# Kernel optimization log

Measured on AMD Instinct MI355X. Metric: run time of the kernel, lower is better.

The kernel has to match this reference:

```python
import jax, jax.numpy as jnp
import numpy as np

C = 256
NUM_HEADS = 8
NUM_GROUPS = 32
EPS = 1e-5


def setup_inputs() -> dict:
    key = jax.random.key(0)
    ks = jax.random.split(key, 7)
    B, H, W = 2, 64, 64
    x = jax.random.normal(ks[0], (B, C, H, W), dtype=jnp.float32)
    norm_gamma = jnp.ones((C,), dtype=jnp.float32)
    norm_beta = jnp.zeros((C,), dtype=jnp.float32)
    # 1x1 convs == per-pixel linear layers; store weights as (out_ch, in_ch)
    qkv_w = jax.random.normal(ks[1], (3 * C, C), dtype=jnp.float32) * (1.0 / np.sqrt(C))
    qkv_b = jnp.zeros((3 * C,), dtype=jnp.float32)
    proj_w = jax.random.normal(ks[2], (C, C), dtype=jnp.float32) * (1.0 / np.sqrt(C))
    proj_b = jnp.zeros((C,), dtype=jnp.float32)
    return {"x": x, "norm_gamma": norm_gamma, "norm_beta": norm_beta,
            "qkv_w": qkv_w, "qkv_b": qkv_b, "proj_w": proj_w, "proj_b": proj_b}


def _group_norm(x, gamma, beta):
    B, Cc, H, W = x.shape
    xg = x.reshape(B, NUM_GROUPS, Cc // NUM_GROUPS, H, W)
    mean = xg.mean(axis=(2, 3, 4), keepdims=True)
    var = xg.var(axis=(2, 3, 4), keepdims=True)
    xn = ((xg - mean) * jax.lax.rsqrt(var + EPS)).reshape(B, Cc, H, W)
    return xn * gamma[None, :, None, None] + beta[None, :, None, None]


def reference(x, norm_gamma, norm_beta, qkv_w, qkv_b, proj_w, proj_b):
    B, Cc, H, W = x.shape
    hd = Cc // NUM_HEADS
    N = H * W

    h = _group_norm(x, norm_gamma, norm_beta)
    # 1x1 conv: (3C,C) x (B,C,H,W) -> (B,3C,H,W)
    qkv = jnp.einsum('oc,bchw->bohw', qkv_w, h) + qkv_b[None, :, None, None]
    q, k, v = jnp.split(qkv, 3, axis=1)

    def heads(t):  # (B,C,H,W) -> (B,heads,N,hd)
        return t.reshape(B, NUM_HEADS, hd, N).transpose(0, 1, 3, 2)

    q, k, v = heads(q), heads(k), heads(v)
    scale = hd ** (-0.5)
    attn = jax.nn.softmax(jnp.einsum('bhnd,bhmd->bhnm', q, k) * scale, axis=-1)
    out = jnp.einsum('bhnm,bhmd->bhnd', attn, v)  # (B,heads,N,hd)
    out = out.transpose(0, 1, 3, 2).reshape(B, Cc, H, W)
    out = jnp.einsum('oc,bchw->bohw', proj_w, out) + proj_b[None, :, None, None]
    return x + out
```

## Files before the change

kernel.cpp:

```cpp
#include <hip/hip_runtime.h>
#include <math.h>

#define C_    256
#define NH    8
#define HD_   32
#define NG    32
#define CPG   8
#define NPIX  4096
#define BATCH 2
#define EPSV  1e-5f
#define SLOG2 0.25503489f
#define MF    16.0f
#define KVB   128
#define KSTR  40
#define VSTR  136
#define KPS2  2048

typedef __bf16 bf16x8 __attribute__((ext_vector_type(8)));
typedef __bf16 bf16x4 __attribute__((ext_vector_type(4)));
typedef float  f32x4  __attribute__((ext_vector_type(4)));

__global__ __launch_bounds__(256) void prep_kernel(const float* __restrict__ x,
                                                   float* __restrict__ partial,
                                                   const float* __restrict__ qw,
                                                   const float* __restrict__ pw,
                                                   __bf16* __restrict__ wbq,
                                                   __bf16* __restrict__ wbp) {
    if (blockIdx.x >= 512) {
        const int i = ((blockIdx.x - 512) * 256 + threadIdx.x) * 4;
        const float* src;
        __bf16* dst;
        int off;
        if (i < 768 * 256) { src = qw; dst = wbq; off = i; }
        else { src = pw; dst = wbp; off = i - 768 * 256; }
        const float4 v = *(const float4*)(src + off);
        bf16x4 o;
        o[0] = (__bf16)v.x; o[1] = (__bf16)v.y; o[2] = (__bf16)v.z; o[3] = (__bf16)v.w;
        *(bf16x4*)(dst + off) = o;
        return;
    }
    const int bg = blockIdx.x >> 3;
    const int part = blockIdx.x & 7;
    const int b = bg >> 5, g = bg & 31;
    const float* __restrict__ xp = x + ((size_t)(b * C_ + g * CPG)) * NPIX;

    float s = 0.f, ss = 0.f;
    #pragma unroll
    for (int p = 0; p < 4; ++p) {
        const int i = part * 4096 + p * 1024 + threadIdx.x * 4;
        const float4 v = *(const float4*)(xp + i);
        s  += v.x + v.y + v.z + v.w;
        ss += v.x * v.x + v.y * v.y + v.z * v.z + v.w * v.w;
    }
    #pragma unroll
    for (int off = 32; off; off >>= 1) {
        s  += __shfl_down(s, off);
        ss += __shfl_down(ss, off);
    }
    __shared__ float ls[4], lss[4];
    const int wid = threadIdx.x >> 6, lane = threadIdx.x & 63;
    if (lane == 0) { ls[wid] = s; lss[wid] = ss; }
    __syncthreads();
    if (threadIdx.x == 0) {
        float S = 0.f, SS = 0.f;
        #pragma unroll
        for (int w = 0; w < 4; ++w) { S += ls[w]; SS += lss[w]; }
        partial[bg * 16 + part * 2 + 0] = S;
        partial[bg * 16 + part * 2 + 1] = SS;
    }
}

__global__ __launch_bounds__(256) void qkv_gemm_kernel(const __bf16* __restrict__ wbq,
                                                       const float* __restrict__ bias,
                                                       const float* __restrict__ x,
                                                       const float* __restrict__ partial,
                                                       const float* __restrict__ gamma,
                                                       const float* __restrict__ beta,
                                                       __bf16* __restrict__ Qb,
                                                       __bf16* __restrict__ Kb,
                                                       __bf16* __restrict__ Vb) {
    const int b = blockIdx.z;
    const int n0 = blockIdx.x * 64;
    __shared__ __align__(16) __bf16 tile[64][264];
    __shared__ float gstat[NG][2];

    if (threadIdx.x < NG) {
        float S = 0.f, SS = 0.f;
        #pragma unroll
        for (int p = 0; p < 8; ++p) {
            S  += partial[(b * NG + threadIdx.x) * 16 + p * 2 + 0];
            SS += partial[(b * NG + threadIdx.x) * 16 + p * 2 + 1];
        }
        const float inv_n = 1.0f / (float)(CPG * NPIX);
        const float mean = S * inv_n;
        const float var  = SS * inv_n - mean * mean;
        gstat[threadIdx.x][0] = mean;
        gstat[threadIdx.x][1] = rsqrtf(var + EPSV);
    }
    __syncthreads();

    {
        const int nn = (threadIdx.x & 15) * 4;
        #pragma unroll
        for (int p = 0; p < 16; ++p) {
            const int c = (threadIdx.x >> 4) + p * 16;
            const float4 v = *(const float4*)(x + ((size_t)(b * C_ + c)) * NPIX + n0 + nn);
            const int g = c >> 3;
            const float ga = gamma[c] * gstat[g][1];
            const float be = beta[c] - gstat[g][0] * ga;
            tile[nn + 0][c] = (__bf16)(v.x * ga + be);
            tile[nn + 1][c] = (__bf16)(v.y * ga + be);
            tile[nn + 2][c] = (__bf16)(v.z * ga + be);
            tile[nn + 3][c] = (__bf16)(v.w * ga + be);
        }
    }
    __syncthreads();

    const int wave = threadIdx.x >> 6, lane = threadIdx.x & 63;
    const int col = lane & 15, g = lane >> 4;
    const int m0 = blockIdx.y * 128 + wave * 32;

    f32x4 acc[2][4];
    #pragma unroll
    for (int i = 0; i < 2; ++i)
        #pragma unroll
        for (int j = 0; j < 4; ++j) acc[i][j] = (f32x4){0.f, 0.f, 0.f, 0.f};

    #pragma unroll
    for (int c0 = 0; c0 < C_; c0 += 32) {
        bf16x8 la[2], lb[4];
        #pragma unroll
        for (int mb = 0; mb < 2; ++mb)
            la[mb] = *(const bf16x8*)(wbq + (size_t)(m0 + mb * 16 + col) * C_ + c0 + g * 8);
        #pragma unroll
        for (int nb = 0; nb < 4; ++nb)
            lb[nb] = *(const bf16x8*)(&tile[nb * 16 + col][c0 + g * 8]);
        #pragma unroll
        for (int mb = 0; mb < 2; ++mb)
            #pragma unroll
            for (int nb = 0; nb < 4; ++nb)
                acc[mb][nb] = __builtin_amdgcn_mfma_f32_16x16x32_bf16(la[mb], lb[nb], acc[mb][nb], 0, 0, 0);
    }

    #pragma unroll
    for (int mb = 0; mb < 2; ++mb) {
        const int mbase = m0 + mb * 16 + 4 * g;
        const float4 b4 = *(const float4*)(bias + mbase);
        const int route = mbase >> 8;
        const int bh = b * NH + ((mbase >> 5) & 7);
        const int d0 = mbase & 31;
        #pragma unroll
        for (int nb = 0; nb < 4; ++nb) {
            const int n = n0 + nb * 16 + col;
            f32x4 v = acc[mb][nb];
            v[0] += b4.x; v[1] += b4.y; v[2] += b4.z; v[3] += b4.w;
            if (route == 0) {
                bf16x4 o;
                #pragma unroll
                for (int r = 0; r < 4; ++r) o[r] = (__bf16)(v[r] * SLOG2);
                *(bf16x4*)(Qb + (((size_t)bh * NPIX + n) << 5) + d0) = o;
            } else if (route == 1) {
                bf16x4 o;
                #pragma unroll
                for (int r = 0; r < 4; ++r) o[r] = (__bf16)v[r];
                *(bf16x4*)(Kb + (((size_t)bh * NPIX + n) << 5) + d0) = o;
            } else {
                #pragma unroll
                for (int r = 0; r < 4; ++r)
                    Vb[((size_t)bh * HD_ + d0 + r) * NPIX + n] = (__bf16)v[r];
            }
        }
    }
}

__global__ __launch_bounds__(512) void attn_kernel(const __bf16* __restrict__ Qb,
                                                   const __bf16* __restrict__ Kb,
                                                   const __bf16* __restrict__ Vb,
                                                   __bf16* __restrict__ aot) {
    __shared__ __align__(16) char smem[75776];
    __bf16 (*Ks)[2][KVB][KSTR] = (__bf16 (*)[2][KVB][KSTR])(smem);
    __bf16 (*Vs)[2][HD_][VSTR] = (__bf16 (*)[2][HD_][VSTR])(smem + 40960);
    float* pbuf = (float*)smem;

    const int id = blockIdx.x;
    const int h = id & 7;
    const int rest = id >> 3;
    const int b = rest >> 5;
    const int qt = rest & 31;

    const int wave = threadIdx.x >> 6, lane = threadIdx.x & 63;
    const int hw = wave >> 2, wv = wave & 3;
    const int col = lane & 15, g = lane >> 4;
    const int bh = b * NH + h;
    const int q0 = qt * 128 + wv * 32;

    const __bf16* __restrict__ qp = Qb + ((size_t)bh * NPIX + q0) * HD_;
    const __bf16* __restrict__ kp = Kb + ((size_t)bh * NPIX + hw * KPS2) * HD_;
    const __bf16* __restrict__ vp = Vb + (size_t)bh * HD_ * NPIX + hw * KPS2;

    const int sk_key = wv * 16 + (lane >> 2);
    const int sk_seg = (lane & 3) * 8;
    const int sv_d   = wv * 8 + (lane >> 3);
    const int sv_seg = (lane & 7) * 8;
    const int vslot  = (sv_seg & 32) + ((((sv_seg & 15) >> 2) << 3)) + (((sv_seg >> 4) & 1) << 2);
    const __bf16* __restrict__ kg = kp + (size_t)sk_key * HD_ + sk_seg;
    const __bf16* __restrict__ vg = vp + (size_t)sv_d * NPIX + sv_seg;

    const bf16x8 fq0 = *(const bf16x8*)(qp + col * HD_ + g * 8);
    const bf16x8 fq1 = *(const bf16x8*)(qp + (16 + col) * HD_ + g * 8);

    bf16x8 ones;
    #pragma unroll
    for (int j = 0; j < 8; ++j) ones[j] = (__bf16)1.0f;
    const f32x4 mfc = {-MF, -MF, -MF, -MF};

    f32x4 acc00 = {0.f,0.f,0.f,0.f}, acc01 = {0.f,0.f,0.f,0.f};
    f32x4 acc10 = {0.f,0.f,0.f,0.f}, acc11 = {0.f,0.f,0.f,0.f};
    f32x4 accL0 = {0.f,0.f,0.f,0.f}, accL1 = {0.f,0.f,0.f,0.f};

    {
        const bf16x8 rk0 = *(const bf16x8*)(kg);
        const bf16x8 rk1 = *(const bf16x8*)(kg + (size_t)64 * HD_);
        const bf16x8 rv0 = *(const bf16x8*)(vg);
        const bf16x8 rv1 = *(const bf16x8*)(vg + 64);
        *(bf16x8*)&Ks[hw][0][sk_key][sk_seg]      = rk0;
        *(bf16x8*)&Ks[hw][0][sk_key + 64][sk_seg] = rk1;
        bf16x4 lo, hi;
        #pragma unroll
        for (int j = 0; j < 4; ++j) { lo[j] = rv0[j]; hi[j] = rv0[4 + j]; }
        *(bf16x4*)&Vs[hw][0][sv_d][vslot]     = lo;
        *(bf16x4*)&Vs[hw][0][sv_d][vslot + 8] = hi;
        #pragma unroll
        for (int j = 0; j < 4; ++j) { lo[j] = rv1[j]; hi[j] = rv1[4 + j]; }
        *(bf16x4*)&Vs[hw][0][sv_d][vslot + 64]     = lo;
        *(bf16x4*)&Vs[hw][0][sv_d][vslot + 64 + 8] = hi;
    }
    __syncthreads();

    const int nt = KPS2 / KVB;
    for (int t = 0; t < nt; ++t) {
        const int cur = t & 1;
        bf16x8 nk0, nk1, nv0, nv1;
        const bool more = (t + 1 < nt);
        {
            const size_t koff = (size_t)(more ? (t + 1) * KVB : 0);
            nk0 = *(const bf16x8*)(kg + koff * HD_);
            nk1 = *(const bf16x8*)(kg + (koff + 64) * HD_);
            nv0 = *(const bf16x8*)(vg + koff);
            nv1 = *(const bf16x8*)(vg + koff + 64);
        }

        #pragma unroll
        for (int kk = 0; kk < KVB; kk += 32) {
            const bf16x8 fk0 = *(const bf16x8*)(&Ks[hw][cur][kk + col][g * 8]);
            const bf16x8 fk1 = *(const bf16x8*)(&Ks[hw][cur][kk + 16 + col][g * 8]);
            const bf16x8 fv0 = *(const bf16x8*)(&Vs[hw][cur][col][kk + 8 * g]);
            const bf16x8 fv1 = *(const bf16x8*)(&Vs[hw][cur][col + 16][kk + 8 * g]);

            __builtin_amdgcn_s_setprio(1);
            f32x4 s00 = __builtin_amdgcn_mfma_f32_16x16x32_bf16(fk0, fq0, mfc, 0, 0, 0);
            f32x4 s10 = __builtin_amdgcn_mfma_f32_16x16x32_bf16(fk1, fq0, mfc, 0, 0, 0);
            f32x4 s01 = __builtin_amdgcn_mfma_f32_16x16x32_bf16(fk0, fq1, mfc, 0, 0, 0);
            f32x4 s11 = __builtin_amdgcn_mfma_f32_16x16x32_bf16(fk1, fq1, mfc, 0, 0, 0);
            __builtin_amdgcn_s_setprio(0);

            float p0[8], p1[8];
            #pragma unroll
            for (int r = 0; r < 4; ++r) {
                p0[r]     = __builtin_amdgcn_exp2f(s00[r]);
                p0[4 + r] = __builtin_amdgcn_exp2f(s10[r]);
                p1[r]     = __builtin_amdgcn_exp2f(s01[r]);
                p1[4 + r] = __builtin_amdgcn_exp2f(s11[r]);
            }

            bf16x8 fp0, fp1;
            #pragma unroll
            for (int j = 0; j < 8; ++j) { fp0[j] = (__bf16)p0[j]; fp1[j] = (__bf16)p1[j]; }

            __builtin_amdgcn_s_setprio(1);
            accL0 = __builtin_amdgcn_mfma_f32_16x16x32_bf16(ones, fp0, accL0, 0, 0, 0);
            accL1 = __builtin_amdgcn_mfma_f32_16x16x32_bf16(ones, fp1, accL1, 0, 0, 0);
            acc00 = __builtin_amdgcn_mfma_f32_16x16x32_bf16(fv0, fp0, acc00, 0, 0, 0);
            acc01 = __builtin_amdgcn_mfma_f32_16x16x32_bf16(fv1, fp0, acc01, 0, 0, 0);
            acc10 = __builtin_amdgcn_mfma_f32_16x16x32_bf16(fv0, fp1, acc10, 0, 0, 0);
            acc11 = __builtin_amdgcn_mfma_f32_16x16x32_bf16(fv1, fp1, acc11, 0, 0, 0);
            __builtin_amdgcn_s_setprio(0);
        }

        if (more) {
            *(bf16x8*)&Ks[hw][cur ^ 1][sk_key][sk_seg]      = nk0;
            *(bf16x8*)&Ks[hw][cur ^ 1][sk_key + 64][sk_seg] = nk1;
            bf16x4 lo, hi;
            #pragma unroll
            for (int j = 0; j < 4; ++j) { lo[j] = nv0[j]; hi[j] = nv0[4 + j]; }
            *(bf16x4*)&Vs[hw][cur ^ 1][sv_d][vslot]     = lo;
            *(bf16x4*)&Vs[hw][cur ^ 1][sv_d][vslot + 8] = hi;
            #pragma unroll
            for (int j = 0; j < 4; ++j) { lo[j] = nv1[j]; hi[j] = nv1[4 + j]; }
            *(bf16x4*)&Vs[hw][cur ^ 1][sv_d][vslot + 64]     = lo;
            *(bf16x4*)&Vs[hw][cur ^ 1][sv_d][vslot + 64 + 8] = hi;
        }
        __syncthreads();
    }

    float l0 = accL0[0], l1 = accL1[0];

    if (hw == 1) {
        float* pp = pbuf + ((size_t)wv * 64 + lane) * 20;
        *(f32x4*)(pp + 0)  = acc00;
        *(f32x4*)(pp + 4)  = acc01;
        *(f32x4*)(pp + 8)  = acc10;
        *(f32x4*)(pp + 12) = acc11;
        pp[16] = l0; pp[17] = l1;
    }
    __syncthreads();
    if (hw == 0) {
        const float* pp = pbuf + ((size_t)wv * 64 + lane) * 20;
        const f32x4 b00 = *(const f32x4*)(pp + 0);
        const f32x4 b01 = *(const f32x4*)(pp + 4);
        const f32x4 b10 = *(const f32x4*)(pp + 8);
        const f32x4 b11 = *(const f32x4*)(pp + 12);
        #pragma unroll
        for (int r = 0; r < 4; ++r) {
            acc00[r] += b00[r]; acc01[r] += b01[r];
            acc10[r] += b10[r]; acc11[r] += b11[r];
        }
        const float inv0 = 1.0f / (l0 + pp[16]);
        const float inv1 = 1.0f / (l1 + pp[17]);
        const int cb = h * HD_ + 4 * g;
        {
            __bf16* op = aot + ((size_t)(b * NPIX) + q0 + col) * C_ + cb;
            bf16x4 o0, o1;
            #pragma unroll
            for (int r = 0; r < 4; ++r) { o0[r] = (__bf16)(acc00[r] * inv0); o1[r] = (__bf16)(acc01[r] * inv0); }
            *(bf16x4*)(op) = o0;
            *(bf16x4*)(op + 16) = o1;
        }
        {
            __bf16* op = aot + ((size_t)(b * NPIX) + q0 + 16 + col) * C_ + cb;
            bf16x4 o0, o1;
            #pragma unroll
            for (int r = 0; r < 4; ++r) { o0[r] = (__bf16)(acc10[r] * inv1); o1[r] = (__bf16)(acc11[r] * inv1); }
            *(bf16x4*)(op) = o0;
            *(bf16x4*)(op + 16) = o1;
        }
    }
}

__global__ __launch_bounds__(256) void proj_gemm_kernel(const __bf16* __restrict__ wbp,
                                                        const float* __restrict__ bias,
                                                        const __bf16* __restrict__ aot,
                                                        const float* __restrict__ x,
                                                        float* __restrict__ out) {
    const int b = blockIdx.z;
    const int wave = threadIdx.x >> 6, lane = threadIdx.x & 63;
    const int col = lane & 15, g = lane >> 4;
    const int n0 = blockIdx.x * 64 + (wave & 1) * 32;
    const int m0 = blockIdx.y * 64 + (wave >> 1) * 32;
    const __bf16* __restrict__ ap = aot + (size_t)b * NPIX * C_;

    f32x4 acc[2][2];
    #pragma unroll
    for (int i = 0; i < 2; ++i)
        #pragma unroll
        for (int j = 0; j < 2; ++j) acc[i][j] = (f32x4){0.f, 0.f, 0.f, 0.f};

    #pragma unroll
    for (int c0 = 0; c0 < C_; c0 += 32) {
        bf16x8 la[2], lb[2];
        #pragma unroll
        for (int mb = 0; mb < 2; ++mb)
            la[mb] = *(const bf16x8*)(wbp + (size_t)(m0 + mb * 16 + col) * C_ + c0 + g * 8);
        #pragma unroll
        for (int nb = 0; nb < 2; ++nb)
            lb[nb] = *(const bf16x8*)(ap + (size_t)(n0 + nb * 16 + col) * C_ + c0 + g * 8);
        #pragma unroll
        for (int mb = 0; mb < 2; ++mb)
            #pragma unroll
            for (int nb = 0; nb < 2; ++nb)
                acc[mb][nb] = __builtin_amdgcn_mfma_f32_16x16x32_bf16(la[mb], lb[nb], acc[mb][nb], 0, 0, 0);
    }

    #pragma unroll
    for (int mb = 0; mb < 2; ++mb) {
        const int mbase = m0 + mb * 16 + 4 * g;
        const float4 b4 = *(const float4*)(bias + mbase);
        const float bias_r[4] = {b4.x, b4.y, b4.z, b4.w};
        #pragma unroll
        for (int nb = 0; nb < 2; ++nb) {
            const int n = n0 + nb * 16 + col;
            #pragma unroll
            for (int r = 0; r < 4; ++r) {
                const size_t idx = ((size_t)(b * C_ + mbase + r)) * NPIX + n;
                out[idx] = acc[mb][nb][r] + bias_r[r] + x[idx];
            }
        }
    }
}

extern "C" void kernel_launch(void* const* d_in, const int* in_sizes, int n_in,
                              void* d_out, int out_size, void* d_ws, size_t ws_size,
                              hipStream_t stream) {
    (void)in_sizes; (void)n_in; (void)out_size; (void)ws_size;
    const float* x      = (const float*)d_in[0];
    const float* gamma  = (const float*)d_in[1];
    const float* beta   = (const float*)d_in[2];
    const float* qkv_w  = (const float*)d_in[3];
    const float* qkv_b  = (const float*)d_in[4];
    const float* proj_w = (const float*)d_in[5];
    const float* proj_b = (const float*)d_in[6];
    float* out = (float*)d_out;

    char* ws = (char*)d_ws;
    __bf16* wbq     = (__bf16*)(ws);
    __bf16* wbp     = (__bf16*)(ws + 0x60000);
    float*  partial = (float*) (ws + 0x80000);
    __bf16* Qb      = (__bf16*)(ws + 0x500000);
    __bf16* Kb      = (__bf16*)(ws + 0x900000);
    __bf16* Vb      = (__bf16*)(ws + 0xD00000);
    __bf16* aot     = (__bf16*)(ws + 0x1100000);

    prep_kernel<<<dim3(768), dim3(256), 0, stream>>>(x, partial, qkv_w, proj_w, wbq, wbp);
    qkv_gemm_kernel<<<dim3(NPIX / 64, 768 / 128, BATCH), dim3(256), 0, stream>>>(
        wbq, qkv_b, x, partial, gamma, beta, Qb, Kb, Vb);
    attn_kernel<<<dim3(32 * NH * BATCH), dim3(512), 0, stream>>>(Qb, Kb, Vb, aot);
    proj_gemm_kernel<<<dim3(NPIX / 64, C_ / 64, BATCH), dim3(256), 0, stream>>>(wbp, proj_b, aot, x, out);
}
```

Baseline: 77.36 us.

## Split attention KV range across two blocks and add combine kernel

The attention kernel now splits each query tile's key range across two blocks, so each block covers a quarter of the keys per half-warpgroup, and the grid doubles from 512 to 1024 blocks. The KV tile shrinks from 128 to 64, which halves shared memory per block and may allow more blocks per CU. Partial normalized outputs and row sums go to a workspace, and a new combine kernel merges them into the head-interleaved layout. This targets low occupancy on a 256-CU device, at the cost of an extra launch, extra global traffic, and an extra bf16 rounding step. Merging the two partials by their row sums is exact only because a fixed max offset is used instead of a per-row running max.

```diff
diff --git a/kernel.cpp b/kernel.cpp
--- a/kernel.cpp
+++ b/kernel.cpp
@@ -11,10 +11,10 @@
 #define EPSV  1e-5f
 #define SLOG2 0.25503489f
 #define MF    16.0f
-#define KVB   128
+#define KVB   64
 #define KSTR  40
-#define VSTR  136
-#define KPS2  2048
+#define VSTR  72
+#define KPS4  1024
 
 typedef __bf16 bf16x8 __attribute__((ext_vector_type(8)));
 typedef __bf16 bf16x4 __attribute__((ext_vector_type(4)));
@@ -176,27 +176,29 @@
 __global__ __launch_bounds__(512) void attn_kernel(const __bf16* __restrict__ Qb,
                                                    const __bf16* __restrict__ Kb,
                                                    const __bf16* __restrict__ Vb,
-                                                   __bf16* __restrict__ aot) {
-    __shared__ __align__(16) char smem[75776];
+                                                   __bf16* __restrict__ po,
+                                                   float* __restrict__ lv) {
+    __shared__ __align__(16) char smem[38912];
     __bf16 (*Ks)[2][KVB][KSTR] = (__bf16 (*)[2][KVB][KSTR])(smem);
-    __bf16 (*Vs)[2][HD_][VSTR] = (__bf16 (*)[2][HD_][VSTR])(smem + 40960);
+    __bf16 (*Vs)[2][HD_][VSTR] = (__bf16 (*)[2][HD_][VSTR])(smem + 20480);
     float* pbuf = (float*)smem;
 
     const int id = blockIdx.x;
-    const int h = id & 7;
-    const int rest = id >> 3;
-    const int b = rest >> 5;
-    const int qt = rest & 31;
+    const int h  = id & 7;
+    const int sp = (id >> 3) & 1;
+    const int b  = (id >> 4) & 1;
+    const int qt = id >> 5;
 
     const int wave = threadIdx.x >> 6, lane = threadIdx.x & 63;
     const int hw = wave >> 2, wv = wave & 3;
     const int col = lane & 15, g = lane >> 4;
     const int bh = b * NH + h;
     const int q0 = qt * 128 + wv * 32;
+    const int kbase = (sp * 2 + hw) * KPS4;
 
     const __bf16* __restrict__ qp = Qb + ((size_t)bh * NPIX + q0) * HD_;
-    const __bf16* __restrict__ kp = Kb + ((size_t)bh * NPIX + hw * KPS2) * HD_;
-    const __bf16* __restrict__ vp = Vb + (size_t)bh * HD_ * NPIX + hw * KPS2;
+    const __bf16* __restrict__ kp = Kb + ((size_t)bh * NPIX + kbase) * HD_;
+    const __bf16* __restrict__ vp = Vb + (size_t)bh * HD_ * NPIX + kbase;
 
     const int sk_key = wv * 16 + (lane >> 2);
     const int sk_seg = (lane & 3) * 8;
@@ -219,35 +221,26 @@
     f32x4 accL0 = {0.f,0.f,0.f,0.f}, accL1 = {0.f,0.f,0.f,0.f};
 
     {
-        const bf16x8 rk0 = *(const bf16x8*)(kg);
-        const bf16x8 rk1 = *(const bf16x8*)(kg + (size_t)64 * HD_);
-        const bf16x8 rv0 = *(const bf16x8*)(vg);
-        const bf16x8 rv1 = *(const bf16x8*)(vg + 64);
-        *(bf16x8*)&Ks[hw][0][sk_key][sk_seg]      = rk0;
-        *(bf16x8*)&Ks[hw][0][sk_key + 64][sk_seg] = rk1;
+        const bf16x8 rk = *(const bf16x8*)(kg);
+        const bf16x8 rv = *(const bf16x8*)(vg);
+        *(bf16x8*)&Ks[hw][0][sk_key][sk_seg] = rk;
         bf16x4 lo, hi;
         #pragma unroll
-        for (int j = 0; j < 4; ++j) { lo[j] = rv0[j]; hi[j] = rv0[4 + j]; }
+        for (int j = 0; j < 4; ++j) { lo[j] = rv[j]; hi[j] = rv[4 + j]; }
         *(bf16x4*)&Vs[hw][0][sv_d][vslot]     = lo;
         *(bf16x4*)&Vs[hw][0][sv_d][vslot + 8] = hi;
-        #pragma unroll
-        for (int j = 0; j < 4; ++j) { lo[j] = rv1[j]; hi[j] = rv1[4 + j]; }
-        *(bf16x4*)&Vs[hw][0][sv_d][vslot + 64]     = lo;
-        *(bf16x4*)&Vs[hw][0][sv_d][vslot + 64 + 8] = hi;
     }
     __syncthreads();
 
-    const int nt = KPS2 / KVB;
+    const int nt = KPS4 / KVB;
     for (int t = 0; t < nt; ++t) {
         const int cur = t & 1;
-        bf16x8 nk0, nk1, nv0, nv1;
+        bf16x8 nk, nv;
         const bool more = (t + 1 < nt);
         {
             const size_t koff = (size_t)(more ? (t + 1) * KVB : 0);
-            nk0 = *(const bf16x8*)(kg + koff * HD_);
-            nk1 = *(const bf16x8*)(kg + (koff + 64) * HD_);
-            nv0 = *(const bf16x8*)(vg + koff);
-            nv1 = *(const bf16x8*)(vg + koff + 64);
+            nk = *(const bf16x8*)(kg + koff * HD_);
+            nv = *(const bf16x8*)(vg + koff);
         }
 
         #pragma unroll
@@ -288,17 +281,12 @@
         }
 
         if (more) {
-            *(bf16x8*)&Ks[hw][cur ^ 1][sk_key][sk_seg]      = nk0;
-            *(bf16x8*)&Ks[hw][cur ^ 1][sk_key + 64][sk_seg] = nk1;
+            *(bf16x8*)&Ks[hw][cur ^ 1][sk_key][sk_seg] = nk;
             bf16x4 lo, hi;
             #pragma unroll
-            for (int j = 0; j < 4; ++j) { lo[j] = nv0[j]; hi[j] = nv0[4 + j]; }
+            for (int j = 0; j < 4; ++j) { lo[j] = nv[j]; hi[j] = nv[4 + j]; }
             *(bf16x4*)&Vs[hw][cur ^ 1][sv_d][vslot]     = lo;
             *(bf16x4*)&Vs[hw][cur ^ 1][sv_d][vslot + 8] = hi;
-            #pragma unroll
-            for (int j = 0; j < 4; ++j) { lo[j] = nv1[j]; hi[j] = nv1[4 + j]; }
-            *(bf16x4*)&Vs[hw][cur ^ 1][sv_d][vslot + 64]     = lo;
-            *(bf16x4*)&Vs[hw][cur ^ 1][sv_d][vslot + 64 + 8] = hi;
         }
         __syncthreads();
     }
@@ -325,11 +313,13 @@
             acc00[r] += b00[r]; acc01[r] += b01[r];
             acc10[r] += b10[r]; acc11[r] += b11[r];
         }
-        const float inv0 = 1.0f / (l0 + pp[16]);
-        const float inv1 = 1.0f / (l1 + pp[17]);
-        const int cb = h * HD_ + 4 * g;
+        const float ls0 = l0 + pp[16];
+        const float ls1 = l1 + pp[17];
+        const float inv0 = 1.0f / ls0;
+        const float inv1 = 1.0f / ls1;
+        const size_t pb = (size_t)(sp * NH * BATCH + bh) * NPIX;
         {
-            __bf16* op = aot + ((size_t)(b * NPIX) + q0 + col) * C_ + cb;
+            __bf16* op = po + (pb + q0 + col) * HD_ + 4 * g;
             bf16x4 o0, o1;
             #pragma unroll
             for (int r = 0; r < 4; ++r) { o0[r] = (__bf16)(acc00[r] * inv0); o1[r] = (__bf16)(acc01[r] * inv0); }
@@ -337,14 +327,39 @@
             *(bf16x4*)(op + 16) = o1;
         }
         {
-            __bf16* op = aot + ((size_t)(b * NPIX) + q0 + 16 + col) * C_ + cb;
+            __bf16* op = po + (pb + q0 + 16 + col) * HD_ + 4 * g;
             bf16x4 o0, o1;
             #pragma unroll
             for (int r = 0; r < 4; ++r) { o0[r] = (__bf16)(acc10[r] * inv1); o1[r] = (__bf16)(acc11[r] * inv1); }
             *(bf16x4*)(op) = o0;
             *(bf16x4*)(op + 16) = o1;
         }
-    }
+        if (g == 0) {
+            lv[pb + q0 + col] = ls0;
+            lv[pb + q0 + 16 + col] = ls1;
+        }
+    }
+}
+
+__global__ __launch_bounds__(256) void combine_kernel(const __bf16* __restrict__ po,
+                                                      const float* __restrict__ lv,
+                                                      __bf16* __restrict__ aot) {
+    const int id = blockIdx.x * 256 + threadIdx.x;
+    const int bh = id >> 15;
+    const int n  = (id >> 3) & (NPIX - 1);
+    const int dblk = id & 7;
+
+    const float l0 = lv[(size_t)bh * NPIX + n];
+    const float l1 = lv[(size_t)(NH * BATCH + bh) * NPIX + n];
+    const float inv = 1.0f / (l0 + l1);
+    const bf16x4 v0 = *(const bf16x4*)(po + ((size_t)bh * NPIX + n) * HD_ + dblk * 4);
+    const bf16x4 v1 = *(const bf16x4*)(po + ((size_t)(NH * BATCH + bh) * NPIX + n) * HD_ + dblk * 4);
+    bf16x4 o;
+    #pragma unroll
+    for (int r = 0; r < 4; ++r)
+        o[r] = (__bf16)((l0 * (float)v0[r] + l1 * (float)v1[r]) * inv);
+    const int b = bh >> 3, h = bh & 7;
+    *(bf16x4*)(aot + ((size_t)(b * NPIX) + n) * C_ + h * HD_ + dblk * 4) = o;
 }
 
 __global__ __launch_bounds__(256) void proj_gemm_kernel(const __bf16* __restrict__ wbp,
@@ -419,10 +434,13 @@
     __bf16* Kb      = (__bf16*)(ws + 0x900000);
     __bf16* Vb      = (__bf16*)(ws + 0xD00000);
     __bf16* aot     = (__bf16*)(ws + 0x1100000);
+    __bf16* po      = (__bf16*)(ws + 0x1500000);
+    float*  lv      = (float*) (ws + 0x1D00000);
 
     prep_kernel<<<dim3(768), dim3(256), 0, stream>>>(x, partial, qkv_w, proj_w, wbq, wbp);
     qkv_gemm_kernel<<<dim3(NPIX / 64, 768 / 128, BATCH), dim3(256), 0, stream>>>(
         wbq, qkv_b, x, partial, gamma, beta, Qb, Kb, Vb);
-    attn_kernel<<<dim3(32 * NH * BATCH), dim3(512), 0, stream>>>(Qb, Kb, Vb, aot);
+    attn_kernel<<<dim3(32 * 2 * NH * BATCH), dim3(512), 0, stream>>>(Qb, Kb, Vb, po, lv);
+    combine_kernel<<<dim3(NH * BATCH * NPIX * 8 / 256), dim3(256), 0, stream>>>(po, lv, aot);
     proj_gemm_kernel<<<dim3(NPIX / 64, C_ / 64, BATCH), dim3(256), 0, stream>>>(wbp, proj_b, aot, x, out);
 }
```

Measured after the change: 79.82 us. 3.2% more time.
